# Kernel tuning notes

Measured on AMD Instinct MI355X. Metric: run time of the kernel, lower is better.

## Reference

```python
import jax, jax.numpy as jnp
import numpy as np

NEG_SLOPE = 0.125


def _ssm_step(u, s, A, Bm, C, D):
    # u: [N,2]; s: [N,2,4,2] (re/im); A,Bm: [2,4,2]; C: [1,2,4,2]; D: [1,2]
    sr, si = s[..., 0], s[..., 1]
    Ar, Ai = A[..., 0], A[..., 1]
    Br, Bi = Bm[..., 0], Bm[..., 1]
    uf = u[..., None]  # [N,2,1]
    # next_state = A * state + B * u  (complex elementwise)
    nr = Ar * sr - Ai * si + Br * uf
    ni = Ar * si + Ai * sr + Bi * uf
    Cr, Ci = C[..., 0], C[..., 1]  # [c=1, h=2, f=4]
    # y = 2 * Re( sum_f C[c,h,f] * next_state[n,h,f] ) -> [N, c, h]
    yr = jnp.einsum('chf,nhf->nch', Cr, nr) - jnp.einsum('chf,nhf->nch', Ci, ni)
    y = 2.0 * yr + u[:, None, :] * D  # [N,1,2]
    y = y.reshape(u.shape[0], 2)  # (c h) flatten with c=1
    ns = jnp.stack([nr, ni], axis=-1)  # [N,2,4,2]
    return y, ns


def _act(x):
    return jnp.where(x >= 0, x, NEG_SLOPE * x)


def setup_inputs() -> dict:
    key = jax.random.key(0)
    ks = jax.random.split(key, 9)
    B = 1048576
    return {
        'x': jax.random.normal(ks[0], (B, 4), dtype=jnp.float32),
        'states': jax.random.normal(ks[1], (4, B, 2, 4, 2), dtype=jnp.float32),
        'fc1_w': jax.random.normal(ks[2], (2, 4), dtype=jnp.float32),
        'fc1_b': jax.random.normal(ks[3], (2,), dtype=jnp.float32),
        'fc_w': jax.random.normal(ks[4], (5, 2, 2), dtype=jnp.float32),
        'fc_b': jax.random.normal(ks[5], (5, 2), dtype=jnp.float32),
        'A': jax.random.normal(ks[6], (4, 2, 4, 2), dtype=jnp.float32),
        'Bm': jax.random.normal(ks[7], (4, 2, 4, 2), dtype=jnp.float32),
        'C': jax.random.normal(ks[8], (4, 1, 2, 4, 2), dtype=jnp.float32),
        'D': jax.random.normal(jax.random.fold_in(key, 99), (4, 1, 2), dtype=jnp.float32),
    }


def reference(x, states, fc1_w, fc1_b, fc_w, fc_b, A, Bm, C, D):
    # fc1 (input layer): [N,4] -> [N,2]
    h = x @ fc1_w.T + fc1_b
    new_states = []
    for i in range(4):
        h, ns = _ssm_step(h, states[i], A[i], Bm[i], C[i], D[i])
        new_states.append(ns)
        h = _act(h)
        h = h @ fc_w[i].T + fc_b[i]
    # fc10
    h = h @ fc_w[4].T + fc_b[4]
    return h, jnp.stack(new_states, axis=0)
```

## Files before the change

### kernel.cpp

```cpp
#include <hip/hip_runtime.h>


constexpr float NEG_SLOPE = 0.125f;

__global__ __launch_bounds__(256) void ssm_fused(
    const float* __restrict__ x,
    const float* __restrict__ states,
    const float* __restrict__ fc1_w,
    const float* __restrict__ fc1_b,
    const float* __restrict__ fc_w,
    const float* __restrict__ fc_b,
    const float* __restrict__ A,
    const float* __restrict__ Bm,
    const float* __restrict__ Cm,
    const float* __restrict__ Dm,
    float* __restrict__ out_h,
    float* __restrict__ out_states,
    int B)
{
    __shared__ float w[240];
    const int t = threadIdx.x;
    if (t < 240) {
        float v;
        if (t < 8)        v = fc1_w[t];
        else if (t < 10)  v = fc1_b[t - 8];
        else if (t < 30)  v = fc_w[t - 10];
        else if (t < 40)  v = fc_b[t - 30];
        else if (t < 104) v = A[t - 40];
        else if (t < 168) v = Bm[t - 104];
        else if (t < 232) v = Cm[t - 168];
        else              v = Dm[t - 232];
        w[t] = v;
    }
    __syncthreads();

    const int n = blockIdx.x * 256 + t;
    if (n >= B) return;

    const float4 xv = ((const float4*)x)[n];
    float h0 = w[8] + xv.x * w[0] + xv.y * w[1] + xv.z * w[2] + xv.w * w[3];
    float h1 = w[9] + xv.x * w[4] + xv.y * w[5] + xv.z * w[6] + xv.w * w[7];

    const float* wA  = w + 40;
    const float* wB  = w + 104;
    const float* wC  = w + 168;
    const float* wD  = w + 232;
    const float* wfc = w + 10;
    const float* wfb = w + 30;

#pragma unroll
    for (int i = 0; i < 4; ++i) {
        const size_t base = ((size_t)i * (size_t)B + (size_t)n) * 16;
        const float4* sp = (const float4*)(states + base);
        const float4 sv0 = sp[0], sv1 = sp[1], sv2 = sp[2], sv3 = sp[3];
        const float s[16] = { sv0.x, sv0.y, sv0.z, sv0.w,
                              sv1.x, sv1.y, sv1.z, sv1.w,
                              sv2.x, sv2.y, sv2.z, sv2.w,
                              sv3.x, sv3.y, sv3.z, sv3.w };
        float ns[16];
        float acc0 = 0.f, acc1 = 0.f;
#pragma unroll
        for (int hh = 0; hh < 2; ++hh) {
            const float u = hh ? h1 : h0;
            float acc = 0.f;
#pragma unroll
            for (int f = 0; f < 4; ++f) {
                const int idx = hh * 8 + f * 2;
                const float Ar = wA[i*16 + idx], Ai = wA[i*16 + idx + 1];
                const float Br = wB[i*16 + idx], Bi = wB[i*16 + idx + 1];
                const float Cr = wC[i*16 + idx], Ci = wC[i*16 + idx + 1];
                const float sr = s[idx], si = s[idx + 1];
                const float nr = Ar * sr - Ai * si + Br * u;
                const float ni = Ar * si + Ai * sr + Bi * u;
                ns[idx]     = nr;
                ns[idx + 1] = ni;
                acc += Cr * nr - Ci * ni;
            }
            if (hh) acc1 = acc; else acc0 = acc;
        }

        float y0 = 2.f * acc0 + h0 * wD[i*2 + 0];
        float y1 = 2.f * acc1 + h1 * wD[i*2 + 1];
        y0 = (y0 >= 0.f) ? y0 : NEG_SLOPE * y0;
        y1 = (y1 >= 0.f) ? y1 : NEG_SLOPE * y1;
        const float nh0 = wfb[i*2 + 0] + wfc[i*4 + 0] * y0 + wfc[i*4 + 1] * y1;
        const float nh1 = wfb[i*2 + 1] + wfc[i*4 + 2] * y0 + wfc[i*4 + 3] * y1;
        h0 = nh0; h1 = nh1;

        float4* op = (float4*)(out_states + base);
        op[0] = make_float4(ns[0],  ns[1],  ns[2],  ns[3]);
        op[1] = make_float4(ns[4],  ns[5],  ns[6],  ns[7]);
        op[2] = make_float4(ns[8],  ns[9],  ns[10], ns[11]);
        op[3] = make_float4(ns[12], ns[13], ns[14], ns[15]);
    }

    const float o0 = wfb[8] + wfc[16] * h0 + wfc[17] * h1;
    const float o1 = wfb[9] + wfc[18] * h0 + wfc[19] * h1;
    ((float2*)out_h)[n] = make_float2(o0, o1);
}

extern "C" void kernel_launch(void* const* d_in, const int* in_sizes, int n_in,
                              void* d_out, int out_size, void* d_ws, size_t ws_size,
                              hipStream_t stream) {
    const float* x      = (const float*)d_in[0];
    const float* states = (const float*)d_in[1];
    const float* fc1_w  = (const float*)d_in[2];
    const float* fc1_b  = (const float*)d_in[3];
    const float* fc_w   = (const float*)d_in[4];
    const float* fc_b   = (const float*)d_in[5];
    const float* A      = (const float*)d_in[6];
    const float* Bm     = (const float*)d_in[7];
    const float* Cm     = (const float*)d_in[8];
    const float* Dm     = (const float*)d_in[9];
    const int B = in_sizes[0] / 4;

    float* out_h      = (float*)d_out;
    float* out_states = (float*)d_out + (size_t)2 * (size_t)B;

    dim3 grid((B + 255) / 256), block(256);
    hipLaunchKernelGGL(ssm_fused, grid, block, 0, stream,
                       x, states, fc1_w, fc1_b, fc_w, fc_b, A, Bm, Cm, Dm,
                       out_h, out_states, B);
}
```

Measured before the change: 489.1 us.

## Split each row across four lanes with shuffle reductions and nontemporal state I/O

Each batch row is now handled by four threads, each owning one 16-byte chunk of the 64-byte state per layer. Partial C-projections are combined with two xor-shuffles. Adjacent lanes therefore touch contiguous memory, giving fully coalesced 16-byte loads and stores where the old code strided 64 bytes per thread. State traffic also uses nontemporal loads and stores. The cost is four times as many threads, with redundant x loads and scalar h math per lane, plus shuffle latency inside the serial layer chain.

```diff
diff --git a/kernel.cpp b/kernel.cpp
--- a/kernel.cpp
+++ b/kernel.cpp
@@ -2,6 +2,8 @@
 
 
 constexpr float NEG_SLOPE = 0.125f;
+
+typedef float fv4 __attribute__((ext_vector_type(4)));
 
 __global__ __launch_bounds__(256) void ssm_fused(
     const float* __restrict__ x,
@@ -18,7 +20,7 @@
     float* __restrict__ out_states,
     int B)
 {
-    __shared__ float w[240];
+    __shared__ __align__(16) float w[240];
     const int t = threadIdx.x;
     if (t < 240) {
         float v;
@@ -34,7 +36,9 @@
     }
     __syncthreads();
 
-    const int n = blockIdx.x * 256 + t;
+    const int g = blockIdx.x * 256 + t;
+    const int n = g >> 2;
+    const int c = g & 3;
     if (n >= B) return;
 
     const float4 xv = ((const float4*)x)[n];
@@ -47,56 +51,45 @@
     const float* wD  = w + 232;
     const float* wfc = w + 10;
     const float* wfb = w + 30;
+    const bool hi = (c & 2) != 0;
 
 #pragma unroll
     for (int i = 0; i < 4; ++i) {
-        const size_t base = ((size_t)i * (size_t)B + (size_t)n) * 16;
-        const float4* sp = (const float4*)(states + base);
-        const float4 sv0 = sp[0], sv1 = sp[1], sv2 = sp[2], sv3 = sp[3];
-        const float s[16] = { sv0.x, sv0.y, sv0.z, sv0.w,
-                              sv1.x, sv1.y, sv1.z, sv1.w,
-                              sv2.x, sv2.y, sv2.z, sv2.w,
-                              sv3.x, sv3.y, sv3.z, sv3.w };
-        float ns[16];
-        float acc0 = 0.f, acc1 = 0.f;
-#pragma unroll
-        for (int hh = 0; hh < 2; ++hh) {
-            const float u = hh ? h1 : h0;
-            float acc = 0.f;
-#pragma unroll
-            for (int f = 0; f < 4; ++f) {
-                const int idx = hh * 8 + f * 2;
-                const float Ar = wA[i*16 + idx], Ai = wA[i*16 + idx + 1];
-                const float Br = wB[i*16 + idx], Bi = wB[i*16 + idx + 1];
-                const float Cr = wC[i*16 + idx], Ci = wC[i*16 + idx + 1];
-                const float sr = s[idx], si = s[idx + 1];
-                const float nr = Ar * sr - Ai * si + Br * u;
-                const float ni = Ar * si + Ai * sr + Bi * u;
-                ns[idx]     = nr;
-                ns[idx + 1] = ni;
-                acc += Cr * nr - Ci * ni;
-            }
-            if (hh) acc1 = acc; else acc0 = acc;
-        }
+        const size_t base = ((size_t)i * (size_t)B + (size_t)n) * 16 + (size_t)(c * 4);
+        const fv4 s  = __builtin_nontemporal_load((const fv4*)(states + base));
+        const fv4 a  = *(const fv4*)(wA + i * 16 + c * 4);
+        const fv4 b  = *(const fv4*)(wB + i * 16 + c * 4);
+        const fv4 cc = *(const fv4*)(wC + i * 16 + c * 4);
 
-        float y0 = 2.f * acc0 + h0 * wD[i*2 + 0];
-        float y1 = 2.f * acc1 + h1 * wD[i*2 + 1];
+        const float u = hi ? h1 : h0;
+        const float nr0 = a.x * s.x - a.y * s.y + b.x * u;
+        const float ni0 = a.x * s.y + a.y * s.x + b.y * u;
+        const float nr1 = a.z * s.z - a.w * s.w + b.z * u;
+        const float ni1 = a.z * s.w + a.w * s.z + b.w * u;
+
+        float part = cc.x * nr0 - cc.y * ni0 + cc.z * nr1 - cc.w * ni1;
+        part += __shfl_xor(part, 1);
+        const float other = __shfl_xor(part, 2);
+        const float acc0 = hi ? other : part;
+        const float acc1 = hi ? part  : other;
+
+        float y0 = 2.f * acc0 + h0 * wD[i * 2 + 0];
+        float y1 = 2.f * acc1 + h1 * wD[i * 2 + 1];
         y0 = (y0 >= 0.f) ? y0 : NEG_SLOPE * y0;
         y1 = (y1 >= 0.f) ? y1 : NEG_SLOPE * y1;
-        const float nh0 = wfb[i*2 + 0] + wfc[i*4 + 0] * y0 + wfc[i*4 + 1] * y1;
-        const float nh1 = wfb[i*2 + 1] + wfc[i*4 + 2] * y0 + wfc[i*4 + 3] * y1;
+        const float nh0 = wfb[i * 2 + 0] + wfc[i * 4 + 0] * y0 + wfc[i * 4 + 1] * y1;
+        const float nh1 = wfb[i * 2 + 1] + wfc[i * 4 + 2] * y0 + wfc[i * 4 + 3] * y1;
         h0 = nh0; h1 = nh1;
 
-        float4* op = (float4*)(out_states + base);
-        op[0] = make_float4(ns[0],  ns[1],  ns[2],  ns[3]);
-        op[1] = make_float4(ns[4],  ns[5],  ns[6],  ns[7]);
-        op[2] = make_float4(ns[8],  ns[9],  ns[10], ns[11]);
-        op[3] = make_float4(ns[12], ns[13], ns[14], ns[15]);
+        fv4 nsv; nsv.x = nr0; nsv.y = ni0; nsv.z = nr1; nsv.w = ni1;
+        __builtin_nontemporal_store(nsv, (fv4*)(out_states + base));
     }
 
-    const float o0 = wfb[8] + wfc[16] * h0 + wfc[17] * h1;
-    const float o1 = wfb[9] + wfc[18] * h0 + wfc[19] * h1;
-    ((float2*)out_h)[n] = make_float2(o0, o1);
+    if (c == 0) {
+        const float o0 = wfb[8] + wfc[16] * h0 + wfc[17] * h1;
+        const float o1 = wfb[9] + wfc[18] * h0 + wfc[19] * h1;
+        ((float2*)out_h)[n] = make_float2(o0, o1);
+    }
 }
 
 extern "C" void kernel_launch(void* const* d_in, const int* in_sizes, int n_in,
@@ -117,7 +110,8 @@
     float* out_h      = (float*)d_out;
     float* out_states = (float*)d_out + (size_t)2 * (size_t)B;
 
-    dim3 grid((B + 255) / 256), block(256);
+    const long long threads = 4LL * (long long)B;
+    dim3 grid((unsigned)((threads + 255) / 256)), block(256);
     hipLaunchKernelGGL(ssm_fused, grid, block, 0, stream,
                        x, states, fc1_w, fc1_b, fc_w, fc_b, A, Bm, Cm, Dm,
                        out_h, out_states, B);
```

Measured after the change: 465.1 us. 1.05x faster.
